# Kernel optimization log

Hardware: AMD Instinct MI355X
Metric: run time of the kernel (lower is better)

The kernel has to match this reference:

```python
import jax, jax.numpy as jnp
import numpy as np

B = 32
T_CAP = 63            # max_caption_length - 1
VOCAB = 32000
IMG_DIM = 20480
EMB = 512
LSTM_DIM = 500


def setup_inputs() -> dict:
    key = jax.random.key(0)
    ks = jax.random.split(key, 10)
    s = 0.02
    return {
        "input_image": jax.random.normal(ks[0], (B, IMG_DIM), dtype=jnp.float32),
        "input_caption": jax.random.randint(ks[1], (B, T_CAP), 0, VOCAB, dtype=jnp.int32),
        # image_embedding Dense
        "W_img": jax.random.normal(ks[2], (IMG_DIM, EMB), dtype=jnp.float32) * s,
        "b_img": jnp.zeros((EMB,), dtype=jnp.float32),
        # caption_embedding table
        "emb": jax.random.normal(ks[3], (VOCAB, EMB), dtype=jnp.float32) * s,
        # LSTM kernels (keras gate order: i, f, c, o)
        "W_lstm": jax.random.normal(ks[4], (EMB, 4 * LSTM_DIM), dtype=jnp.float32) * s,
        "U_lstm": jax.random.normal(ks[5], (LSTM_DIM, 4 * LSTM_DIM), dtype=jnp.float32) * s,
        "b_lstm": jnp.concatenate([jnp.zeros((LSTM_DIM,)), jnp.ones((LSTM_DIM,)),
                                    jnp.zeros((2 * LSTM_DIM,))]).astype(jnp.float32),  # unit forget bias
        # output Dense + softmax
        "W_out": jax.random.normal(ks[6], (LSTM_DIM, VOCAB), dtype=jnp.float32) * s,
        "b_out": jnp.zeros((VOCAB,), dtype=jnp.float32),
    }


def _lstm_scan(x, W, U, b):
    # x: [B, T, EMB] -> outputs [B, T, LSTM_DIM]
    Bx = x.shape[0]
    # precompute input projections for all timesteps (one big GEMM)
    xz = jnp.einsum('btd,dg->btg', x, W) + b  # [B, T, 4H]
    xz = jnp.swapaxes(xz, 0, 1)               # [T, B, 4H]
    h0 = jnp.zeros((Bx, LSTM_DIM), dtype=x.dtype)
    c0 = jnp.zeros((Bx, LSTM_DIM), dtype=x.dtype)

    def step(carry, z_t):
        h, c = carry
        z = z_t + h @ U                        # [B, 4H]
        i, f, g, o = jnp.split(z, 4, axis=-1)  # keras gate order i,f,c,o
        i = jax.nn.sigmoid(i)
        f = jax.nn.sigmoid(f)
        g = jnp.tanh(g)
        o = jax.nn.sigmoid(o)
        c_new = f * c + i * g
        h_new = o * jnp.tanh(c_new)
        return (h_new, c_new), h_new

    _, hs = jax.lax.scan(step, (h0, c0), xz)   # hs: [T, B, H]
    return jnp.swapaxes(hs, 0, 1)


def reference(input_image, input_caption, W_img, b_img, emb, W_lstm, U_lstm, b_lstm, W_out, b_out):
    # image embedding -> one leading timestep
    x_image = (input_image @ W_img + b_img)[:, None, :]      # [B, 1, EMB]
    x_caption = emb[input_caption]                            # [B, T-1, EMB]
    x = jnp.concatenate([x_image, x_caption], axis=1)         # [B, T, EMB]
    h = _lstm_scan(x, W_lstm, U_lstm, b_lstm)                 # [B, T, H]
    logits = jnp.einsum('bth,hv->btv', h, W_out) + b_out      # [B, T, VOCAB]
    return jax.nn.softmax(logits, axis=-1)
```

## Files before the change

kernel.cpp:

```cpp
#include <hip/hip_runtime.h>

typedef float f32x4 __attribute__((ext_vector_type(4)));
typedef short s16x8 __attribute__((ext_vector_type(8)));
typedef unsigned int u32;
typedef unsigned long long u64;

#define B_    32
#define T_    64
#define TCAP_ 63
#define V_    32000
#define IMGD_ 20480
#define E_    512
#define H_    500
#define KP_   512

#define OFF_X      0ul
#define OFF_XZ     4194304ul
#define OFF_HPAD   20578304ul
#define OFF_HS     20643840ul
#define OFF_UPREP  22740992ul
#define OFF_WT     24838144ul
#define OFF_RS     57606144ul

__device__ __forceinline__ short bf16rn(float f) {
  u32 u = __float_as_uint(f);
  u += 0x7fff + ((u >> 16) & 1);
  return (short)(u >> 16);
}
__device__ __forceinline__ float sigf(float x) {
  return 1.0f / (1.0f + __expf(-x));
}
__device__ __forceinline__ void gload_lds16(const void* g, void* l) {
  __builtin_amdgcn_global_load_lds((const __attribute__((address_space(1))) void*)g,
                                   (__attribute__((address_space(3))) void*)l, 16, 0, 0);
}

__global__ __launch_bounds__(256) void k_init(const float* __restrict__ bimg,
                                              const float* __restrict__ emb,
                                              const int* __restrict__ cap,
                                              float* __restrict__ x,
                                              u32* __restrict__ hpad_u32,
                                              float* __restrict__ rowsum,
                                              u32* __restrict__ flags) {
  int i = blockIdx.x * 256 + threadIdx.x;
  if (i < 262144) {
    int m = i >> 7, j4 = i & 127;
    int b = m >> 6, t = m & 63;
    f32x4 v;
    if (t == 0) v = *(const f32x4*)(bimg + j4 * 4);
    else {
      int r = cap[b * TCAP_ + (t - 1)];
      v = *(const f32x4*)(emb + (size_t)r * E_ + j4 * 4);
    }
    *(f32x4*)(x + (size_t)m * E_ + j4 * 4) = v;
  } else if (i < 262144 + 16384) {
    hpad_u32[i - 262144] = 0u;
  } else if (i < 262144 + 16384 + 512) {
    int k = i - 262144 - 16384;
    *(f32x4*)(rowsum + k * 4) = (f32x4){0.f, 0.f, 0.f, 0.f};
  } else if (i < 262144 + 16384 + 512 + 32) {
    flags[i - (262144 + 16384 + 512)] = 0u;
  }
}

__global__ __launch_bounds__(256) void k_img(const float* __restrict__ img,
                                             const float* __restrict__ W,
                                             float* __restrict__ x) {
  __shared__ float simg[32][128];
  int ct = blockIdx.x & 7;
  int ks = blockIdx.x >> 3;
  int tid = threadIdx.x;
  int j = tid & 63, bq = tid >> 6;
  int col = ct * 64 + j;
  float acc[8] = {0.f, 0.f, 0.f, 0.f, 0.f, 0.f, 0.f, 0.f};
  int kbeg = ks * 1280;
  for (int k0 = kbeg; k0 < kbeg + 1280; k0 += 128) {
    __syncthreads();
    for (int u = tid; u < 32 * 32; u += 256) {
      int b = u >> 5, kq = (u & 31) * 4;
      *(f32x4*)&simg[b][kq] = *(const f32x4*)(img + (size_t)b * IMGD_ + k0 + kq);
    }
    __syncthreads();
    for (int k = 0; k < 128; ++k) {
      float w = W[(size_t)(k0 + k) * E_ + col];
#pragma unroll
      for (int r = 0; r < 8; ++r) acc[r] += simg[bq * 8 + r][k] * w;
    }
  }
#pragma unroll
  for (int r = 0; r < 8; ++r) {
    int b = bq * 8 + r;
    atomicAdd(x + (size_t)b * T_ * E_ + col, acc[r]);
  }
}

__global__ __launch_bounds__(256) void k_xz(const float* __restrict__ A,
                                            const float* __restrict__ Wl,
                                            const float* __restrict__ bl,
                                            float* __restrict__ xz) {
  __shared__ float sA[32][68];
  __shared__ float sB[32][68];
  int mt = blockIdx.x & 31, nt = blockIdx.x >> 5;
  int m0 = mt * 64, n0 = nt * 64;
  int tid = threadIdx.x;
  int tx = tid & 15, ty = tid >> 4;
  float acc[4][4] = {};
  for (int kb = 0; kb < 512; kb += 32) {
    __syncthreads();
    for (int u = tid; u < 512; u += 256) {
      int r = u >> 3, kq = (u & 7) * 4;
      f32x4 v = *(const f32x4*)(A + (size_t)(m0 + r) * E_ + kb + kq);
      sA[kq + 0][r] = v.x; sA[kq + 1][r] = v.y; sA[kq + 2][r] = v.z; sA[kq + 3][r] = v.w;
    }
    for (int u = tid; u < 512; u += 256) {
      int kk = u >> 4, nj = (u & 15) * 4;
      int n = n0 + nj;
      f32x4 v = (f32x4){0.f, 0.f, 0.f, 0.f};
      if (n < 2000) v = *(const f32x4*)(Wl + (size_t)(kb + kk) * 2000 + n);
      *(f32x4*)&sB[kk][nj] = v;
    }
    __syncthreads();
    for (int k = 0; k < 32; ++k) {
      f32x4 a4 = *(const f32x4*)&sA[k][ty * 4];
      f32x4 b4 = *(const f32x4*)&sB[k][tx * 4];
#pragma unroll
      for (int i = 0; i < 4; ++i)
#pragma unroll
        for (int jj = 0; jj < 4; ++jj) acc[i][jj] += a4[i] * b4[jj];
    }
  }
#pragma unroll
  for (int i = 0; i < 4; ++i) {
    int m = m0 + ty * 4 + i;
    int b = m >> 6, t = m & 63;
#pragma unroll
    for (int jj = 0; jj < 4; ++jj) {
      int n = n0 + tx * 4 + jj;
      if (n < 2000)
        xz[((size_t)t * B_ + b) * 2000 + n] = acc[i][jj] + bl[n];
    }
  }
}

__global__ __launch_bounds__(256) void k_uprep(const float* __restrict__ U,
                                               short* __restrict__ up) {
  int idx = blockIdx.x * 256 + threadIdx.x;
  int k = idx & 511;
  int c = (idx >> 9) & 63;
  int wg = idx >> 15;
  int q = c >> 4, dl = c & 15, dg = wg * 16 + dl;
  float v = 0.f;
  if (dg < H_ && k < H_) v = U[(size_t)k * 2000 + q * H_ + dg];
  up[idx] = bf16rn(v);
}

__global__ __launch_bounds__(256) void k_wt(const float* __restrict__ Wo,
                                            short* __restrict__ Wt) {
  __shared__ float s[32][65];
  int nt = blockIdx.x % 500, kt = blockIdx.x / 500;
  int n0 = nt * 64, k0 = kt * 32;
  int tid = threadIdx.x;
  for (int u = tid; u < 2048; u += 256) {
    int kl = u >> 6, nl = u & 63;
    int k = k0 + kl;
    s[kl][nl] = (k < H_) ? Wo[(size_t)k * V_ + n0 + nl] : 0.f;
  }
  __syncthreads();
  for (int u = tid; u < 2048; u += 256) {
    int nl = u >> 5, kl = u & 31;
    Wt[(size_t)(n0 + nl) * KP_ + k0 + kl] = bf16rn(s[kl][nl]);
  }
}

__global__ __launch_bounds__(128) void k_scan(const short* __restrict__ up,
                                              const float* __restrict__ xz,
                                              short* hpad,
                                              short* __restrict__ hs,
                                              u32* flags) {
  __shared__ short Ul[64 * 512];
  int wg = blockIdx.x;
  int tid = threadIdx.x;
  int lane = tid & 63, mtile = tid >> 6;
  int dl = lane & 15, g16 = lane >> 4;

  const short* usrc = up + (size_t)wg * 64 * 512;
  for (int u = tid; u < 4096; u += 128) {
    int c = u >> 6, kq = (u & 63) * 8;
    u32 off = ((u32)(c * 512 + kq) * 2) ^ ((u32)(c & 7) << 4);
    *(s16x8*)((char*)Ul + off) = *(const s16x8*)(usrc + c * 512 + kq);
  }
  __syncthreads();

  int dg = wg * 16 + dl;
  bool dvalid = dg < H_;
  float cst[4] = {0.f, 0.f, 0.f, 0.f};
  int brow = mtile * 16 + dl;

  float xzr[4][4];
  auto pf = [&](int t) {
#pragma unroll
    for (int q = 0; q < 4; ++q)
#pragma unroll
      for (int reg = 0; reg < 4; ++reg) {
        int b = mtile * 16 + g16 * 4 + reg;
        xzr[q][reg] = dvalid ? xz[((size_t)t * B_ + b) * 2000 + q * 500 + dg] : 0.f;
      }
  };
  pf(0);

  for (int t = 0; t < 64; ++t) {
    f32x4 acc[4];
#pragma unroll
    for (int q = 0; q < 4; ++q) acc[q] = (f32x4){0.f, 0.f, 0.f, 0.f};

    if (t > 0) {
      const short* hsrc = hpad + (size_t)(t & 1) * (B_ * KP_);
      u64 q0[16], q1[16];
#pragma unroll
      for (int kk = 0; kk < 16; ++kk) {
        const u64* p = (const u64*)(hsrc + brow * KP_ + kk * 32 + g16 * 8);
        q0[kk] = __hip_atomic_load(p,     __ATOMIC_RELAXED, __HIP_MEMORY_SCOPE_AGENT);
        q1[kk] = __hip_atomic_load(p + 1, __ATOMIC_RELAXED, __HIP_MEMORY_SCOPE_AGENT);
      }
#pragma unroll
      for (int kk = 0; kk < 16; ++kk) {
        union { s16x8 v; u64 q[2]; } fr;
        fr.q[0] = q0[kk]; fr.q[1] = q1[kk];
#pragma unroll
        for (int q = 0; q < 4; ++q) {
          int c = q * 16 + dl;
          u32 off = ((u32)(c * 512 + kk * 32 + g16 * 8) * 2) ^ ((u32)(c & 7) << 4);
          s16x8 bfr = *(const s16x8*)((const char*)Ul + off);
          acc[q] = __builtin_amdgcn_mfma_f32_16x16x32_bf16(fr.v, bfr, acc[q], 0, 0, 0);
        }
      }
    }

    short hb4[4];
#pragma unroll
    for (int reg = 0; reg < 4; ++reg) {
      float zi = acc[0][reg] + xzr[0][reg];
      float zf = acc[1][reg] + xzr[1][reg];
      float zc = acc[2][reg] + xzr[2][reg];
      float zo = acc[3][reg] + xzr[3][reg];
      float ig = sigf(zi), fg = sigf(zf), gt = tanhf(zc), og = sigf(zo);
      float cn = fg * cst[reg] + ig * gt;
      cst[reg] = cn;
      float h = og * tanhf(cn);
      if (!dvalid) h = 0.f;
      hb4[reg] = bf16rn(h);
    }

    short* hnext = hpad + (size_t)((t + 1) & 1) * (B_ * KP_);
#pragma unroll
    for (int reg = 0; reg < 4; ++reg) {
      int mine = (int)(u32)(unsigned short)hb4[reg];
      int oth = __shfl_xor(mine, 1);
      if ((dl & 1) == 0) {
        int b = mtile * 16 + g16 * 4 + reg;
        u32 val = ((u32)mine) | ((u32)oth << 16);
        __hip_atomic_store((u32*)hnext + ((b * KP_ + dg) >> 1), val,
                           __ATOMIC_RELAXED, __HIP_MEMORY_SCOPE_AGENT);
      }
    }

    if (t < 63) {
      __syncthreads();
      if (tid == 0)
        __hip_atomic_store(&flags[wg], (u32)(t + 1),
                           __ATOMIC_RELAXED, __HIP_MEMORY_SCOPE_AGENT);
      asm volatile("" ::: "memory");
#pragma unroll
      for (int reg = 0; reg < 4; ++reg) {
        int b = mtile * 16 + g16 * 4 + reg;
        hs[((size_t)b * T_ + t) * KP_ + dg] = hb4[reg];
      }
      pf(t + 1);
      if (tid < 64) {
        u32 target = (u32)(t + 1);
        int slot = tid & 31;
        while (true) {
          u32 v = __hip_atomic_load(&flags[slot], __ATOMIC_RELAXED,
                                    __HIP_MEMORY_SCOPE_AGENT);
          if (__all(v >= target)) break;
          __builtin_amdgcn_s_sleep(1);
        }
      }
      __syncthreads();
    } else {
#pragma unroll
      for (int reg = 0; reg < 4; ++reg) {
        int b = mtile * 16 + g16 * 4 + reg;
        hs[((size_t)b * T_ + t) * KP_ + dg] = hb4[reg];
      }
    }
  }
}

template <int PHASE>
__global__ __launch_bounds__(256) void k_gemm(const short* __restrict__ A,
                                              const short* __restrict__ Bt,
                                              const float* __restrict__ bout,
                                              float* __restrict__ out,
                                              float* __restrict__ rowsum) {
  __shared__ short sA[2][128 * 64];
  __shared__ short sB[2][128 * 64];
  int bid = blockIdx.x;
  int mt = bid & 15, nt = bid >> 4;
  int m0 = mt * 128, n0 = nt * 128;
  int tid = threadIdx.x;
  int lane = tid & 63, w = tid >> 6;
  int wr = w >> 1, wc = w & 1;
  int l15 = lane & 15, l4 = lane >> 4;

  f32x4 acc[4][4];
#pragma unroll
  for (int i = 0; i < 4; ++i)
#pragma unroll
    for (int j = 0; j < 4; ++j) acc[i][j] = (f32x4){0.f, 0.f, 0.f, 0.f};

  auto stage = [&](int kc, int buf) {
    const short* ga = A + (size_t)m0 * KP_ + kc * 64;
    const short* gb = Bt + (size_t)n0 * KP_ + kc * 64;
#pragma unroll
    for (int i = 0; i < 4; ++i) {
      int ch = tid + i * 256;
      int rr = ch >> 3, kq = (ch & 7) * 8;
      gload_lds16(ga + (size_t)rr * KP_ + kq, &sA[buf][rr * 64 + kq]);
      gload_lds16(gb + (size_t)rr * KP_ + kq, &sB[buf][rr * 64 + kq]);
    }
  };

  stage(0, 0);
  __syncthreads();
  int buf = 0;
  for (int kc = 0; kc < 8; ++kc) {
    if (kc < 7) stage(kc + 1, buf ^ 1);
#pragma unroll
    for (int k2 = 0; k2 < 2; ++k2) {
      int kloc = k2 * 32 + l4 * 8;
      s16x8 af[4], bfr[4];
#pragma unroll
      for (int fm = 0; fm < 4; ++fm)
        af[fm] = *(const s16x8*)&sA[buf][(wr * 64 + fm * 16 + l15) * 64 + kloc];
#pragma unroll
      for (int fn = 0; fn < 4; ++fn)
        bfr[fn] = *(const s16x8*)&sB[buf][(wc * 64 + fn * 16 + l15) * 64 + kloc];
#pragma unroll
      for (int fm = 0; fm < 4; ++fm)
#pragma unroll
        for (int fn = 0; fn < 4; ++fn)
          acc[fm][fn] = __builtin_amdgcn_mfma_f32_16x16x32_bf16(af[fm], bfr[fn], acc[fm][fn], 0, 0, 0);
    }
    __syncthreads();
    buf ^= 1;
  }

  float bo4[4];
#pragma unroll
  for (int fn = 0; fn < 4; ++fn) bo4[fn] = bout[n0 + wc * 64 + fn * 16 + l15];

#pragma unroll
  for (int fm = 0; fm < 4; ++fm) {
#pragma unroll
    for (int reg = 0; reg < 4; ++reg) {
      int m = m0 + wr * 64 + fm * 16 + l4 * 4 + reg;
      if constexpr (PHASE == 0) {
        float s = 0.f;
#pragma unroll
        for (int fn = 0; fn < 4; ++fn) {
          float e = __expf(acc[fm][fn][reg] + bo4[fn]);
          s += e;
        }
        s += __shfl_xor(s, 1);
        s += __shfl_xor(s, 2);
        s += __shfl_xor(s, 4);
        s += __shfl_xor(s, 8);
        if (l15 == 0) atomicAdd(&rowsum[m], s);
      } else {
        float inv = 1.0f / rowsum[m];
#pragma unroll
        for (int fn = 0; fn < 4; ++fn) {
          int n = n0 + wc * 64 + fn * 16 + l15;
          float e = __expf(acc[fm][fn][reg] + bo4[fn]);
          out[(size_t)m * V_ + n] = e * inv;
        }
      }
    }
  }
}

extern "C" void kernel_launch(void* const* d_in, const int* in_sizes, int n_in,
                              void* d_out, int out_size, void* d_ws, size_t ws_size,
                              hipStream_t stream) {
  const float* img  = (const float*)d_in[0];
  const int*   cap  = (const int*)  d_in[1];
  const float* Wimg = (const float*)d_in[2];
  const float* bimg = (const float*)d_in[3];
  const float* emb  = (const float*)d_in[4];
  const float* Wl   = (const float*)d_in[5];
  const float* Ulm  = (const float*)d_in[6];
  const float* bl   = (const float*)d_in[7];
  const float* Wo   = (const float*)d_in[8];
  const float* bo   = (const float*)d_in[9];
  float* out = (float*)d_out;
  char* ws = (char*)d_ws;

  float* x      = (float*)(ws + OFF_X);
  float* xz     = (float*)(ws + OFF_XZ);
  short* hpad   = (short*)(ws + OFF_HPAD);
  short* hs     = (short*)(ws + OFF_HS);
  short* uprep  = (short*)(ws + OFF_UPREP);
  short* wt     = (short*)(ws + OFF_WT);
  float* rowsum = (float*)(ws + OFF_RS);
  u32*   flags  = (u32*)d_out;

  k_init<<<1090, 256, 0, stream>>>(bimg, emb, cap, x, (u32*)hpad, rowsum, flags);
  k_uprep<<<4096, 256, 0, stream>>>(Ulm, uprep);
  k_wt<<<8000, 256, 0, stream>>>(Wo, wt);
  k_img<<<128, 256, 0, stream>>>(img, Wimg, x);
  k_xz<<<1024, 256, 0, stream>>>(x, Wl, bl, xz);

  {
    const short* up_p = uprep;
    const float* xz_p = xz;
    short* hpad_p = hpad;
    short* hs_p = hs;
    u32* flags_p = flags;
    void* args[] = {&up_p, &xz_p, &hpad_p, &hs_p, &flags_p};
    hipLaunchCooperativeKernel((void*)k_scan, dim3(32), dim3(128), args, 0, stream);
  }

  k_gemm<0><<<4000, 256, 0, stream>>>(hs, wt, bo, out, rowsum);
  k_gemm<1><<<4000, 256, 0, stream>>>(hs, wt, bo, out, rowsum);
}
```

Baseline: 838.3 us.

## Fuse prep kernels, move input projection to bf16 MFMA, per-wave scan flags

```diff
diff --git a/kernel.cpp b/kernel.cpp
--- a/kernel.cpp
+++ b/kernel.cpp
@@ -14,14 +14,16 @@
 #define H_    500
 #define KP_   512
 
-#define OFF_X      0ul
-#define OFF_XZ     4194304ul
+#define OFF_XZ     0ul
+#define OFF_XB     16384000ul
+#define OFF_WLT    18481152ul
 #define OFF_HPAD   20578304ul
 #define OFF_HS     20643840ul
 #define OFF_UPREP  22740992ul
 #define OFF_WT     24838144ul
 #define OFF_RS     57606144ul
 
+
 __device__ __forceinline__ short bf16rn(float f) {
   u32 u = __float_as_uint(f);
   u += 0x7fff + ((u >> 16) & 1);
@@ -35,37 +37,89 @@
                                    (__attribute__((address_space(3))) void*)l, 16, 0, 0);
 }
 
-__global__ __launch_bounds__(256) void k_init(const float* __restrict__ bimg,
+#define PR0 523
+#define PR1 4619
+#define PR2 12619
+#define PR3 13131
+__global__ __launch_bounds__(256) void k_prep(const float* __restrict__ bimg,
                                               const float* __restrict__ emb,
                                               const int* __restrict__ cap,
-                                              float* __restrict__ x,
-                                              u32* __restrict__ hpad_u32,
+                                              const float* __restrict__ U,
+                                              const float* __restrict__ Wo,
+                                              const float* __restrict__ Wl,
+                                              short* __restrict__ xb,
+                                              float* __restrict__ x32,
                                               float* __restrict__ rowsum,
-                                              u32* __restrict__ flags) {
-  int i = blockIdx.x * 256 + threadIdx.x;
-  if (i < 262144) {
-    int m = i >> 7, j4 = i & 127;
-    int b = m >> 6, t = m & 63;
-    f32x4 v;
-    if (t == 0) v = *(const f32x4*)(bimg + j4 * 4);
-    else {
-      int r = cap[b * TCAP_ + (t - 1)];
-      v = *(const f32x4*)(emb + (size_t)r * E_ + j4 * 4);
-    }
-    *(f32x4*)(x + (size_t)m * E_ + j4 * 4) = v;
-  } else if (i < 262144 + 16384) {
-    hpad_u32[i - 262144] = 0u;
-  } else if (i < 262144 + 16384 + 512) {
-    int k = i - 262144 - 16384;
-    *(f32x4*)(rowsum + k * 4) = (f32x4){0.f, 0.f, 0.f, 0.f};
-  } else if (i < 262144 + 16384 + 512 + 32) {
-    flags[i - (262144 + 16384 + 512)] = 0u;
+                                              u32* __restrict__ flags,
+                                              short* __restrict__ up,
+                                              short* __restrict__ wt,
+                                              short* __restrict__ wlt) {
+  __shared__ float s[32][65];
+  int bid = blockIdx.x, tid = threadIdx.x;
+  if (bid < 504) {
+    int u = bid * 256 + tid;
+    int r = u >> 6, j8 = u & 63;
+    int b = r / 63, tt = r - b * 63;
+    int e = cap[b * TCAP_ + tt];
+    const float* src = emb + (size_t)e * E_ + j8 * 8;
+    f32x4 v0 = *(const f32x4*)src;
+    f32x4 v1 = *(const f32x4*)(src + 4);
+    s16x8 o;
+    o[0]=bf16rn(v0.x); o[1]=bf16rn(v0.y); o[2]=bf16rn(v0.z); o[3]=bf16rn(v0.w);
+    o[4]=bf16rn(v1.x); o[5]=bf16rn(v1.y); o[6]=bf16rn(v1.z); o[7]=bf16rn(v1.w);
+    *(s16x8*)(xb + (size_t)(b * T_ + tt + 1) * KP_ + j8 * 8) = o;
+  } else if (bid < 520) {
+    int i = (bid - 504) * 256 + tid;
+    int b = i >> 7, j = i & 127;
+    *(f32x4*)(x32 + b * E_ + j * 4) = *(const f32x4*)(bimg + j * 4);
+  } else if (bid < 522) {
+    int i = (bid - 520) * 256 + tid;
+    *(f32x4*)(rowsum + i * 4) = (f32x4){0.f, 0.f, 0.f, 0.f};
+  } else if (bid < PR0) {
+    if (tid < 64) flags[tid] = 0u;
+  } else if (bid < PR1) {
+    int idx = (bid - PR0) * 256 + tid;
+    int k = idx & 511;
+    int c = (idx >> 9) & 127;
+    int wg = idx >> 16;
+    int q = c >> 5, rem = c & 31, dg = wg * 32 + rem;
+    float v = 0.f;
+    if (dg < H_ && k < H_) v = U[(size_t)k * 2000 + q * H_ + dg];
+    up[idx] = bf16rn(v);
+  } else if (bid < PR2) {
+    int r = bid - PR1;
+    int nt = r % 500, kt = r / 500;
+    int n0 = nt * 64, k0 = kt * 32;
+    for (int u = tid; u < 2048; u += 256) {
+      int kl = u >> 6, nl = u & 63;
+      int k = k0 + kl;
+      s[kl][nl] = (k < H_) ? Wo[(size_t)k * V_ + n0 + nl] : 0.f;
+    }
+    __syncthreads();
+    for (int u = tid; u < 2048; u += 256) {
+      int nl = u >> 5, kl = u & 31;
+      wt[(size_t)(n0 + nl) * KP_ + k0 + kl] = bf16rn(s[kl][nl]);
+    }
+  } else {
+    int r = bid - PR2;
+    int nt = r & 31, kt = r >> 5;
+    int n0 = nt * 64, k0 = kt * 32;
+    for (int u = tid; u < 2048; u += 256) {
+      int kl = u >> 6, nl = u & 63;
+      int n = n0 + nl;
+      s[kl][nl] = (n < 2000) ? Wl[(size_t)(k0 + kl) * 2000 + n] : 0.f;
+    }
+    __syncthreads();
+    for (int u = tid; u < 2048; u += 256) {
+      int nl = u >> 5, kl = u & 31;
+      wlt[(size_t)(n0 + nl) * KP_ + k0 + kl] = bf16rn(s[kl][nl]);
+    }
   }
 }
 
 __global__ __launch_bounds__(256) void k_img(const float* __restrict__ img,
                                              const float* __restrict__ W,
-                                             float* __restrict__ x) {
+                                             float* __restrict__ x32) {
   __shared__ float simg[32][128];
   int ct = blockIdx.x & 7;
   int ks = blockIdx.x >> 3;
@@ -88,110 +142,126 @@
     }
   }
 #pragma unroll
-  for (int r = 0; r < 8; ++r) {
-    int b = bq * 8 + r;
-    atomicAdd(x + (size_t)b * T_ * E_ + col, acc[r]);
-  }
-}
-
-__global__ __launch_bounds__(256) void k_xz(const float* __restrict__ A,
-                                            const float* __restrict__ Wl,
-                                            const float* __restrict__ bl,
-                                            float* __restrict__ xz) {
-  __shared__ float sA[32][68];
-  __shared__ float sB[32][68];
-  int mt = blockIdx.x & 31, nt = blockIdx.x >> 5;
-  int m0 = mt * 64, n0 = nt * 64;
+  for (int r = 0; r < 8; ++r)
+    atomicAdd(x32 + (bq * 8 + r) * E_ + col, acc[r]);
+}
+
+__global__ __launch_bounds__(256) void k_xb(const float* __restrict__ x32,
+                                            short* __restrict__ xb) {
+  int u = blockIdx.x * 256 + threadIdx.x;
+  int b = u >> 6, j8 = u & 63;
+  const float* src = x32 + b * E_ + j8 * 8;
+  f32x4 v0 = *(const f32x4*)src;
+  f32x4 v1 = *(const f32x4*)(src + 4);
+  s16x8 o;
+  o[0]=bf16rn(v0.x); o[1]=bf16rn(v0.y); o[2]=bf16rn(v0.z); o[3]=bf16rn(v0.w);
+  o[4]=bf16rn(v1.x); o[5]=bf16rn(v1.y); o[6]=bf16rn(v1.z); o[7]=bf16rn(v1.w);
+  *(s16x8*)(xb + (size_t)(b * T_) * KP_ + j8 * 8) = o;
+}
+
+__global__ __launch_bounds__(256) void k_xzm(const short* __restrict__ A,
+                                             const short* __restrict__ Bt,
+                                             const float* __restrict__ bl,
+                                             float* __restrict__ xz) {
+  __shared__ short sA[2][128 * 64];
+  __shared__ short sB[2][128 * 64];
+  int bid = blockIdx.x;
+  int mt = bid & 15, nt = bid >> 4;
+  int m0 = mt * 128, n0 = nt * 128;
   int tid = threadIdx.x;
-  int tx = tid & 15, ty = tid >> 4;
-  float acc[4][4] = {};
-  for (int kb = 0; kb < 512; kb += 32) {
-    __syncthreads();
-    for (int u = tid; u < 512; u += 256) {
-      int r = u >> 3, kq = (u & 7) * 4;
-      f32x4 v = *(const f32x4*)(A + (size_t)(m0 + r) * E_ + kb + kq);
-      sA[kq + 0][r] = v.x; sA[kq + 1][r] = v.y; sA[kq + 2][r] = v.z; sA[kq + 3][r] = v.w;
-    }
-    for (int u = tid; u < 512; u += 256) {
-      int kk = u >> 4, nj = (u & 15) * 4;
-      int n = n0 + nj;
-      f32x4 v = (f32x4){0.f, 0.f, 0.f, 0.f};
-      if (n < 2000) v = *(const f32x4*)(Wl + (size_t)(kb + kk) * 2000 + n);
-      *(f32x4*)&sB[kk][nj] = v;
-    }
-    __syncthreads();
-    for (int k = 0; k < 32; ++k) {
-      f32x4 a4 = *(const f32x4*)&sA[k][ty * 4];
-      f32x4 b4 = *(const f32x4*)&sB[k][tx * 4];
-#pragma unroll
-      for (int i = 0; i < 4; ++i)
-#pragma unroll
-        for (int jj = 0; jj < 4; ++jj) acc[i][jj] += a4[i] * b4[jj];
-    }
-  }
-#pragma unroll
-  for (int i = 0; i < 4; ++i) {
-    int m = m0 + ty * 4 + i;
-    int b = m >> 6, t = m & 63;
-#pragma unroll
-    for (int jj = 0; jj < 4; ++jj) {
-      int n = n0 + tx * 4 + jj;
-      if (n < 2000)
-        xz[((size_t)t * B_ + b) * 2000 + n] = acc[i][jj] + bl[n];
-    }
-  }
-}
-
-__global__ __launch_bounds__(256) void k_uprep(const float* __restrict__ U,
-                                               short* __restrict__ up) {
-  int idx = blockIdx.x * 256 + threadIdx.x;
-  int k = idx & 511;
-  int c = (idx >> 9) & 63;
-  int wg = idx >> 15;
-  int q = c >> 4, dl = c & 15, dg = wg * 16 + dl;
-  float v = 0.f;
-  if (dg < H_ && k < H_) v = U[(size_t)k * 2000 + q * H_ + dg];
-  up[idx] = bf16rn(v);
-}
-
-__global__ __launch_bounds__(256) void k_wt(const float* __restrict__ Wo,
-                                            short* __restrict__ Wt) {
-  __shared__ float s[32][65];
-  int nt = blockIdx.x % 500, kt = blockIdx.x / 500;
-  int n0 = nt * 64, k0 = kt * 32;
-  int tid = threadIdx.x;
-  for (int u = tid; u < 2048; u += 256) {
-    int kl = u >> 6, nl = u & 63;
-    int k = k0 + kl;
-    s[kl][nl] = (k < H_) ? Wo[(size_t)k * V_ + n0 + nl] : 0.f;
-  }
+  int lane = tid & 63, w = tid >> 6;
+  int wr = w >> 1, wc = w & 1;
+  int l15 = lane & 15, l4 = lane >> 4;
+
+  f32x4 acc[4][4];
+#pragma unroll
+  for (int i = 0; i < 4; ++i)
+#pragma unroll
+    for (int j = 0; j < 4; ++j) acc[i][j] = (f32x4){0.f, 0.f, 0.f, 0.f};
+
+  auto stage = [&](int kc, int buf) {
+    const short* ga = A + (size_t)m0 * KP_ + kc * 64;
+    const short* gb = Bt + (size_t)n0 * KP_ + kc * 64;
+#pragma unroll
+    for (int i = 0; i < 4; ++i) {
+      int ch = tid + i * 256;
+      int rr = ch >> 3, kq = (ch & 7) * 8;
+      gload_lds16(ga + (size_t)rr * KP_ + kq, &sA[buf][rr * 64 + kq]);
+      gload_lds16(gb + (size_t)rr * KP_ + kq, &sB[buf][rr * 64 + kq]);
+    }
+  };
+
+  stage(0, 0);
   __syncthreads();
-  for (int u = tid; u < 2048; u += 256) {
-    int nl = u >> 5, kl = u & 31;
-    Wt[(size_t)(n0 + nl) * KP_ + k0 + kl] = bf16rn(s[kl][nl]);
-  }
-}
-
-__global__ __launch_bounds__(128) void k_scan(const short* __restrict__ up,
+  int buf = 0;
+  for (int kc = 0; kc < 8; ++kc) {
+    if (kc < 7) stage(kc + 1, buf ^ 1);
+#pragma unroll
+    for (int k2 = 0; k2 < 2; ++k2) {
+      int kloc = k2 * 32 + l4 * 8;
+      s16x8 af[4], bfr[4];
+#pragma unroll
+      for (int fm = 0; fm < 4; ++fm)
+        af[fm] = *(const s16x8*)&sA[buf][(wr * 64 + fm * 16 + l15) * 64 + kloc];
+#pragma unroll
+      for (int fn = 0; fn < 4; ++fn)
+        bfr[fn] = *(const s16x8*)&sB[buf][(wc * 64 + fn * 16 + l15) * 64 + kloc];
+#pragma unroll
+      for (int fm = 0; fm < 4; ++fm)
+#pragma unroll
+        for (int fn = 0; fn < 4; ++fn)
+          acc[fm][fn] = __builtin_amdgcn_mfma_f32_16x16x32_bf16(af[fm], bfr[fn], acc[fm][fn], 0, 0, 0);
+    }
+    __syncthreads();
+    buf ^= 1;
+  }
+
+  float bln[4];
+#pragma unroll
+  for (int fn = 0; fn < 4; ++fn) {
+    int n = n0 + wc * 64 + fn * 16 + l15;
+    bln[fn] = (n < 2000) ? bl[n] : 0.f;
+  }
+#pragma unroll
+  for (int fm = 0; fm < 4; ++fm) {
+#pragma unroll
+    for (int reg = 0; reg < 4; ++reg) {
+      int m = m0 + wr * 64 + fm * 16 + l4 * 4 + reg;
+      int b = m >> 6, t = m & 63;
+#pragma unroll
+      for (int fn = 0; fn < 4; ++fn) {
+        int n = n0 + wc * 64 + fn * 16 + l15;
+        if (n < 2000)
+          xz[((size_t)t * B_ + b) * 2000 + n] = acc[fm][fn][reg] + bln[fn];
+      }
+    }
+  }
+}
+
+__global__ __launch_bounds__(256) void k_scan(const short* __restrict__ up,
                                               const float* __restrict__ xz,
                                               short* hpad,
                                               short* __restrict__ hs,
                                               u32* flags) {
-  __shared__ short Ul[64 * 512];
+  __shared__ short Ul[128 * 512];
   int wg = blockIdx.x;
   int tid = threadIdx.x;
-  int lane = tid & 63, mtile = tid >> 6;
+  int lane = tid & 63;
+  int wv = tid >> 6;
+  int mtile = wv & 1;
+  int dgrp = wv >> 1;
+  int wid = wg * 4 + wv;
   int dl = lane & 15, g16 = lane >> 4;
 
-  const short* usrc = up + (size_t)wg * 64 * 512;
-  for (int u = tid; u < 4096; u += 128) {
+  const short* usrc = up + (size_t)wg * (128 * 512);
+  for (int u = tid; u < 8192; u += 256) {
     int c = u >> 6, kq = (u & 63) * 8;
     u32 off = ((u32)(c * 512 + kq) * 2) ^ ((u32)(c & 7) << 4);
     *(s16x8*)((char*)Ul + off) = *(const s16x8*)(usrc + c * 512 + kq);
   }
   __syncthreads();
 
-  int dg = wg * 16 + dl;
+  int dg = wg * 32 + dgrp * 16 + dl;
   bool dvalid = dg < H_;
   float cst[4] = {0.f, 0.f, 0.f, 0.f};
   int brow = mtile * 16 + dl;
@@ -214,6 +284,11 @@
     for (int q = 0; q < 4; ++q) acc[q] = (f32x4){0.f, 0.f, 0.f, 0.f};
 
     if (t > 0) {
+      u32 target = (u32)t;
+      u32 v = __hip_atomic_load(&flags[lane], __ATOMIC_RELAXED, __HIP_MEMORY_SCOPE_AGENT);
+      while (!__all(v >= target))
+        v = __hip_atomic_load(&flags[lane], __ATOMIC_RELAXED, __HIP_MEMORY_SCOPE_AGENT);
+
       const short* hsrc = hpad + (size_t)(t & 1) * (B_ * KP_);
       u64 q0[16], q1[16];
 #pragma unroll
@@ -228,7 +303,7 @@
         fr.q[0] = q0[kk]; fr.q[1] = q1[kk];
 #pragma unroll
         for (int q = 0; q < 4; ++q) {
-          int c = q * 16 + dl;
+          int c = q * 32 + dgrp * 16 + dl;
           u32 off = ((u32)(c * 512 + kk * 32 + g16 * 8) * 2) ^ ((u32)(c & 7) << 4);
           s16x8 bfr = *(const s16x8*)((const char*)Ul + off);
           acc[q] = __builtin_amdgcn_mfma_f32_16x16x32_bf16(fr.v, bfr, acc[q], 0, 0, 0);
@@ -265,28 +340,16 @@
     }
 
     if (t < 63) {
-      __syncthreads();
-      if (tid == 0)
-        __hip_atomic_store(&flags[wg], (u32)(t + 1),
+      asm volatile("s_waitcnt vmcnt(0)" ::: "memory");
+      if (lane == 0)
+        __hip_atomic_store(&flags[wid], (u32)(t + 1),
                            __ATOMIC_RELAXED, __HIP_MEMORY_SCOPE_AGENT);
-      asm volatile("" ::: "memory");
 #pragma unroll
       for (int reg = 0; reg < 4; ++reg) {
         int b = mtile * 16 + g16 * 4 + reg;
         hs[((size_t)b * T_ + t) * KP_ + dg] = hb4[reg];
       }
       pf(t + 1);
-      if (tid < 64) {
-        u32 target = (u32)(t + 1);
-        int slot = tid & 31;
-        while (true) {
-          u32 v = __hip_atomic_load(&flags[slot], __ATOMIC_RELAXED,
-                                    __HIP_MEMORY_SCOPE_AGENT);
-          if (__all(v >= target)) break;
-          __builtin_amdgcn_s_sleep(1);
-        }
-      }
-      __syncthreads();
     } else {
 #pragma unroll
       for (int reg = 0; reg < 4; ++reg) {
@@ -368,10 +431,8 @@
       if constexpr (PHASE == 0) {
         float s = 0.f;
 #pragma unroll
-        for (int fn = 0; fn < 4; ++fn) {
-          float e = __expf(acc[fm][fn][reg] + bo4[fn]);
-          s += e;
-        }
+        for (int fn = 0; fn < 4; ++fn)
+          s += __expf(acc[fm][fn][reg] + bo4[fn]);
         s += __shfl_xor(s, 1);
         s += __shfl_xor(s, 2);
         s += __shfl_xor(s, 4);
@@ -406,20 +467,22 @@
   float* out = (float*)d_out;
   char* ws = (char*)d_ws;
 
-  float* x      = (float*)(ws + OFF_X);
   float* xz     = (float*)(ws + OFF_XZ);
+  short* xb     = (short*)(ws + OFF_XB);
+  short* wlt    = (short*)(ws + OFF_WLT);
   short* hpad   = (short*)(ws + OFF_HPAD);
   short* hs     = (short*)(ws + OFF_HS);
   short* uprep  = (short*)(ws + OFF_UPREP);
   short* wt     = (short*)(ws + OFF_WT);
   float* rowsum = (float*)(ws + OFF_RS);
   u32*   flags  = (u32*)d_out;
-
-  k_init<<<1090, 256, 0, stream>>>(bimg, emb, cap, x, (u32*)hpad, rowsum, flags);
-  k_uprep<<<4096, 256, 0, stream>>>(Ulm, uprep);
-  k_wt<<<8000, 256, 0, stream>>>(Wo, wt);
-  k_img<<<128, 256, 0, stream>>>(img, Wimg, x);
-  k_xz<<<1024, 256, 0, stream>>>(x, Wl, bl, xz);
+  float* x32    = (float*)d_out + 1024;
+
+  k_prep<<<PR3, 256, 0, stream>>>(bimg, emb, cap, Ulm, Wo, Wl,
+                                  xb, x32, rowsum, flags, uprep, wt, wlt);
+  k_img<<<128, 256, 0, stream>>>(img, Wimg, x32);
+  k_xb<<<8, 256, 0, stream>>>(x32, xb);
+  k_xzm<<<256, 256, 0, stream>>>(xb, wlt, bl, xz);
 
   {
     const short* up_p = uprep;
@@ -428,7 +491,7 @@
     short* hs_p = hs;
     u32* flags_p = flags;
     void* args[] = {&up_p, &xz_p, &hpad_p, &hs_p, &flags_p};
-    hipLaunchCooperativeKernel((void*)k_scan, dim3(32), dim3(128), args, 0, stream);
+    hipLaunchCooperativeKernel((void*)k_scan, dim3(16), dim3(256), args, 0, stream);
   }
 
   k_gemm<0><<<4000, 256, 0, stream>>>(hs, wt, bo, out, rowsum);
```

New measurement: 972.3 us. 16.0% more time.
